# Optimization experiments

Measured on AMD Instinct MI355X. Metric: run time of the kernel, lower is better.

Reference implementation:

```python
import jax, jax.numpy as jnp
import numpy as np

ALPHA = 0.2          # LeakyReLU negative slope
NEG_BIG = -9e15      # zero_vec value used before softmax masking


def setup_inputs() -> dict:
    key = jax.random.key(0)
    k1, k2, k3, k4, k5 = jax.random.split(key, 5)
    N, M, F, K = 2048, 8192, 1024, 10
    feature_matrix = jax.random.normal(k1, (N, F), dtype=jnp.float32)
    embed_matrix = jax.random.normal(k2, (M, F), dtype=jnp.float32)
    # Xavier-ish scaling for params
    weight = jax.random.normal(k3, (F, F), dtype=jnp.float32) * (1.0 / np.sqrt(F))
    a = jax.random.normal(k4, (2 * F, 1), dtype=jnp.float32) * (1.0 / np.sqrt(2 * F))
    neigh_idx = jax.random.randint(k5, (N, K), 0, M, dtype=jnp.int64)
    return {
        "feature_matrix": feature_matrix,
        "embed_matrix": embed_matrix,
        "weight": weight,
        "a": a,
        "neigh_idx": neigh_idx,
    }


def reference(feature_matrix, embed_matrix, weight, a, neigh_idx):
    # feature_matrix: [N, F] features of batch nodes
    # embed_matrix:   [M, F] features of unique sampled neighbors
    # neigh_idx:      [N, K] sampled neighbor columns (set semantics: dups collapse)
    N, F = feature_matrix.shape
    M = embed_matrix.shape[0]
    rows = jnp.arange(N)[:, None]
    mask = jnp.zeros((N, M), dtype=feature_matrix.dtype).at[rows, neigh_idx].set(1.0)

    # GAT kernel path
    hf = feature_matrix @ weight          # [N, F]
    he = embed_matrix @ weight            # [M, F]
    # e_ij = leakyrelu([h_i || h_j] . a) == leakyrelu(h_i.a1 + h_j.a2)
    a1 = a[:F, 0]
    a2 = a[F:, 0]
    e = (hf @ a1)[:, None] + (he @ a2)[None, :]          # [N, M]
    e = jnp.where(e > 0, e, ALPHA * e)                   # LeakyReLU(0.2)
    scores = jnp.where(mask > 0, e, NEG_BIG)
    attention = jax.nn.softmax(scores, axis=1)           # row softmax
    to_feats = attention @ he                            # [N, F]
    return to_feats
```

## Files before the change

### kernel.cpp

```cpp
#include <hip/hip_runtime.h>
#include <math.h>

#define ALPHA 0.2f
#define MAXK 10

typedef _Float16 half8 __attribute__((ext_vector_type(8)));
typedef _Float16 half4 __attribute__((ext_vector_type(4)));
typedef float f32x4 __attribute__((ext_vector_type(4)));

__device__ __forceinline__ void gload_lds16(const void* g, void* l) {
    __builtin_amdgcn_global_load_lds(
        (const __attribute__((address_space(1))) unsigned int*)g,
        (__attribute__((address_space(3))) unsigned int*)l, 16, 0, 0);
}

__global__ void wa_kernel(const float* __restrict__ W, const float* __restrict__ a,
                          float* __restrict__ wa, int F) {
    int wave = (int)((blockIdx.x * blockDim.x + threadIdx.x) >> 6);
    int lane = threadIdx.x & 63;
    if (wave >= F) return;
    const float4* wr = reinterpret_cast<const float4*>(W + (size_t)wave * F);
    const float4* a1 = reinterpret_cast<const float4*>(a);
    const float4* a2 = reinterpret_cast<const float4*>(a + F);
    float acc1 = 0.f, acc2 = 0.f;
    int F4 = F >> 2;
    for (int c = lane; c < F4; c += 64) {
        float4 w = wr[c];
        float4 x = a1[c];
        float4 y = a2[c];
        acc1 += w.x * x.x + w.y * x.y + w.z * x.z + w.w * x.w;
        acc2 += w.x * y.x + w.y * y.y + w.z * y.z + w.w * y.w;
    }
    #pragma unroll
    for (int off = 32; off; off >>= 1) {
        acc1 += __shfl_down(acc1, off);
        acc2 += __shfl_down(acc2, off);
    }
    if (lane == 0) { wa[wave] = acc1; wa[F + wave] = acc2; }
}

__global__ void wt_kernel(const float* __restrict__ W, _Float16* __restrict__ Wt, int F) {
    __shared__ float t[32][33];
    int bx = blockIdx.x * 32;
    int by = blockIdx.y * 32;
    int x = threadIdx.x;
    for (int i = threadIdx.y; i < 32; i += 8)
        t[i][x] = W[(size_t)(bx + i) * F + by + x];
    __syncthreads();
    for (int i = threadIdx.y; i < 32; i += 8)
        Wt[(size_t)(by + i) * F + bx + x] = (_Float16)t[x][i];
}

__global__ __launch_bounds__(256) void aggregate_fused_kernel(
    const float* __restrict__ feat, const float* __restrict__ embed,
    const int* __restrict__ nidx, const float* __restrict__ wa,
    _Float16* __restrict__ agg, int F) {
    const int i = blockIdx.x;
    const int tid = threadIdx.x;
    const int f = tid * 4;

    int idx[MAXK];
    bool dup[MAXK];
    #pragma unroll
    for (int k = 0; k < MAXK; k++) idx[k] = nidx[i * MAXK + k];
    #pragma unroll
    for (int k = 0; k < MAXK; k++) {
        bool d = false;
        #pragma unroll
        for (int p = 0; p < MAXK; p++)
            if (p < k) d |= (idx[p] == idx[k]);
        dup[k] = d;
    }

    float4 wa1 = *(const float4*)&wa[f];
    float4 wa2 = *(const float4*)&wa[F + f];
    float4 fv  = *(const float4*)&feat[(size_t)i * F + f];
    float a1p = fv.x * wa1.x + fv.y * wa1.y + fv.z * wa1.z + fv.w * wa1.w;

    float4 rv[MAXK];
    float a2p[MAXK];
    #pragma unroll
    for (int k = 0; k < MAXK; k++) {
        rv[k] = *(const float4*)&embed[(size_t)idx[k] * F + f];
        a2p[k] = rv[k].x * wa2.x + rv[k].y * wa2.y + rv[k].z * wa2.z + rv[k].w * wa2.w;
    }

    #pragma unroll
    for (int off = 32; off; off >>= 1) {
        a1p += __shfl_down(a1p, off);
        #pragma unroll
        for (int k = 0; k < MAXK; k++) a2p[k] += __shfl_down(a2p[k], off);
    }
    __shared__ float red[MAXK + 1][4];
    const int w = tid >> 6, l = tid & 63;
    if (l == 0) {
        red[0][w] = a1p;
        #pragma unroll
        for (int k = 0; k < MAXK; k++) red[k + 1][w] = a2p[k];
    }
    __syncthreads();

    float s1 = red[0][0] + red[0][1] + red[0][2] + red[0][3];
    float sc[MAXK];
    float m = -INFINITY;
    #pragma unroll
    for (int k = 0; k < MAXK; k++) {
        float v = s1 + red[k + 1][0] + red[k + 1][1] + red[k + 1][2] + red[k + 1][3];
        v = v > 0.f ? v : ALPHA * v;
        sc[k] = v;
        if (!dup[k]) m = fmaxf(m, v);
    }
    float sum = 0.f;
    #pragma unroll
    for (int k = 0; k < MAXK; k++) {
        sc[k] = dup[k] ? 0.f : expf(sc[k] - m);
        sum += sc[k];
    }
    float inv = 1.0f / sum;

    float4 o = make_float4(0.f, 0.f, 0.f, 0.f);
    #pragma unroll
    for (int k = 0; k < MAXK; k++) {
        float wk = sc[k] * inv;
        o.x += wk * rv[k].x;
        o.y += wk * rv[k].y;
        o.z += wk * rv[k].z;
        o.w += wk * rv[k].w;
    }
    half4 h = { (_Float16)o.x, (_Float16)o.y, (_Float16)o.z, (_Float16)o.w };
    *(half4*)&agg[(size_t)i * F + f] = h;
}

__global__ __launch_bounds__(256) void gemm_f16_kernel(
    const _Float16* __restrict__ A, const _Float16* __restrict__ Bt,
    float* __restrict__ C, int M, int N, int K) {
    __shared__ _Float16 As[2][64 * 64];
    __shared__ _Float16 Bs[2][64 * 64];
    const int tid = threadIdx.x;
    const int m0 = blockIdx.y * 64;
    const int n0 = blockIdx.x * 64;
    const int l = tid & 63, wv = tid >> 6;
    const int wm = wv >> 1, wn = wv & 1;
    const int lrow = l & 15, kc = l >> 4;

    const int srow = l >> 3;
    const int sslot = (l & 7) ^ (srow & 7);
    const int nt = K >> 6;

    f32x4 acc[2][2] = {};

    const int rg0 = wv * 2, rg1 = wv * 2 + 1;

    #define STAGE(buf, t)                                                          \
    do {                                                                           \
        int k0_ = (t) * 64;                                                        \
        gload_lds16(&A[(size_t)(m0 + rg0 * 8 + srow) * K + k0_ + sslot * 8],       \
                    (void*)((char*)&As[buf][0] + rg0 * 1024 + l * 16));            \
        gload_lds16(&A[(size_t)(m0 + rg1 * 8 + srow) * K + k0_ + sslot * 8],       \
                    (void*)((char*)&As[buf][0] + rg1 * 1024 + l * 16));            \
        gload_lds16(&Bt[(size_t)(n0 + rg0 * 8 + srow) * K + k0_ + sslot * 8],      \
                    (void*)((char*)&Bs[buf][0] + rg0 * 1024 + l * 16));            \
        gload_lds16(&Bt[(size_t)(n0 + rg1 * 8 + srow) * K + k0_ + sslot * 8],      \
                    (void*)((char*)&Bs[buf][0] + rg1 * 1024 + l * 16));            \
    } while (0)

    STAGE(0, 0);
    asm volatile("s_waitcnt vmcnt(0)" ::: "memory");
    __syncthreads();

    int buf = 0;
    for (int t = 0; t < nt; ++t) {
        if (t + 1 < nt) STAGE(buf ^ 1, t + 1);

        half8 av[2][2], bv[2][2];
        #pragma unroll
        for (int ks = 0; ks < 2; ks++) {
            #pragma unroll
            for (int fq = 0; fq < 2; fq++) {
                int arow = wm * 32 + fq * 16 + lrow;
                int aslot = (ks * 4 + kc) ^ (arow & 7);
                av[ks][fq] = *(const half8*)((const char*)&As[buf][0] + arow * 128 + aslot * 16);
                int brow = wn * 32 + fq * 16 + lrow;
                int bslot = (ks * 4 + kc) ^ (brow & 7);
                bv[ks][fq] = *(const half8*)((const char*)&Bs[buf][0] + brow * 128 + bslot * 16);
            }
        }
        #pragma unroll
        for (int ks = 0; ks < 2; ks++)
            #pragma unroll
            for (int fq = 0; fq < 2; fq++)
                #pragma unroll
                for (int g = 0; g < 2; g++)
                    acc[fq][g] = __builtin_amdgcn_mfma_f32_16x16x32_f16(
                        av[ks][fq], bv[ks][g], acc[fq][g], 0, 0, 0);

        asm volatile("s_waitcnt vmcnt(0)" ::: "memory");
        __syncthreads();
        buf ^= 1;
    }
    #undef STAGE

    #pragma unroll
    for (int fq = 0; fq < 2; fq++)
        #pragma unroll
        for (int g = 0; g < 2; g++)
            #pragma unroll
            for (int r = 0; r < 4; r++)
                C[(size_t)(m0 + wm * 32 + fq * 16 + kc * 4 + r) * N
                  + n0 + wn * 32 + g * 16 + lrow] = acc[fq][g][r];
}

extern "C" void kernel_launch(void* const* d_in, const int* in_sizes, int n_in,
                              void* d_out, int out_size, void* d_ws, size_t ws_size,
                              hipStream_t stream) {
    const float* feat  = (const float*)d_in[0];
    const float* embed = (const float*)d_in[1];
    const float* W     = (const float*)d_in[2];
    const float* a     = (const float*)d_in[3];
    const int*   nidx  = (const int*)d_in[4];

    int F = in_sizes[3] / 2;
    int N = in_sizes[0] / F;
    int M = in_sizes[1] / F;

    float* ws = (float*)d_ws;
    float* wa = ws;
    _Float16* agg_f16 = (_Float16*)(wa + 2 * F);
    _Float16* wt_f16  = agg_f16 + (size_t)N * F;
    (void)M;

    wa_kernel<<<(F * 64 + 255) / 256, 256, 0, stream>>>(W, a, wa, F);
    {
        dim3 grid(F / 32, F / 32), block(32, 8);
        wt_kernel<<<grid, block, 0, stream>>>(W, wt_f16, F);
    }
    aggregate_fused_kernel<<<N, 256, 0, stream>>>(feat, embed, nidx, wa, agg_f16, F);
    {
        dim3 grid(F / 64, N / 64);
        gemm_f16_kernel<<<grid, 256, 0, stream>>>(agg_f16, wt_f16, (float*)d_out, N, F, F);
    }
}
```

Before: 41.41 us.

## Fuse W·a into transpose kernel and enlarge GEMM tile to 128x64 with XCD remap

Folds the W·a reduction into the W transpose kernel. Partial dot products are reduced with 32-lane shuffles and accumulated with atomics after a memset, which removes one kernel launch and a second full read of W. The f16 GEMM tile grows from 64x64 to 128x64, so each wave holds 4x2 MFMA accumulators for more A/B reuse per LDS load. Blocks are also remapped round-robin across 8 XCDs for L2 locality. Costs are float atomics, whose summation order is nondeterministic, higher register and LDS use, and half as many GEMM blocks (256).

```diff
diff --git a/kernel.cpp b/kernel.cpp
--- a/kernel.cpp
+++ b/kernel.cpp
@@ -14,41 +14,31 @@
         (__attribute__((address_space(3))) unsigned int*)l, 16, 0, 0);
 }
 
-__global__ void wa_kernel(const float* __restrict__ W, const float* __restrict__ a,
-                          float* __restrict__ wa, int F) {
-    int wave = (int)((blockIdx.x * blockDim.x + threadIdx.x) >> 6);
-    int lane = threadIdx.x & 63;
-    if (wave >= F) return;
-    const float4* wr = reinterpret_cast<const float4*>(W + (size_t)wave * F);
-    const float4* a1 = reinterpret_cast<const float4*>(a);
-    const float4* a2 = reinterpret_cast<const float4*>(a + F);
-    float acc1 = 0.f, acc2 = 0.f;
-    int F4 = F >> 2;
-    for (int c = lane; c < F4; c += 64) {
-        float4 w = wr[c];
-        float4 x = a1[c];
-        float4 y = a2[c];
-        acc1 += w.x * x.x + w.y * x.y + w.z * x.z + w.w * x.w;
-        acc2 += w.x * y.x + w.y * y.y + w.z * y.z + w.w * y.w;
-    }
-    #pragma unroll
-    for (int off = 32; off; off >>= 1) {
-        acc1 += __shfl_down(acc1, off);
-        acc2 += __shfl_down(acc2, off);
-    }
-    if (lane == 0) { wa[wave] = acc1; wa[F + wave] = acc2; }
-}
-
-__global__ void wt_kernel(const float* __restrict__ W, _Float16* __restrict__ Wt, int F) {
+__global__ void wawt_kernel(const float* __restrict__ W, const float* __restrict__ a,
+                            _Float16* __restrict__ Wt, float* __restrict__ wa, int F) {
     __shared__ float t[32][33];
-    int bx = blockIdx.x * 32;
-    int by = blockIdx.y * 32;
-    int x = threadIdx.x;
-    for (int i = threadIdx.y; i < 32; i += 8)
+    const int bx = blockIdx.x * 32;
+    const int by = blockIdx.y * 32;
+    const int x = threadIdx.x, y = threadIdx.y;
+    for (int i = y; i < 32; i += 8)
         t[i][x] = W[(size_t)(bx + i) * F + by + x];
     __syncthreads();
-    for (int i = threadIdx.y; i < 32; i += 8)
+    for (int i = y; i < 32; i += 8)
         Wt[(size_t)(by + i) * F + bx + x] = (_Float16)t[x][i];
+    float a1 = a[by + x], a2 = a[F + by + x];
+    for (int i = y; i < 32; i += 8) {
+        float w = t[i][x];
+        float p1 = w * a1, p2 = w * a2;
+        #pragma unroll
+        for (int off = 16; off; off >>= 1) {
+            p1 += __shfl_down(p1, off, 32);
+            p2 += __shfl_down(p2, off, 32);
+        }
+        if (x == 0) {
+            atomicAdd(&wa[bx + i], p1);
+            atomicAdd(&wa[F + bx + i], p2);
+        }
+    }
 }
 
 __global__ __launch_bounds__(256) void aggregate_fused_kernel(
@@ -134,34 +124,41 @@
 __global__ __launch_bounds__(256) void gemm_f16_kernel(
     const _Float16* __restrict__ A, const _Float16* __restrict__ Bt,
     float* __restrict__ C, int M, int N, int K) {
-    __shared__ _Float16 As[2][64 * 64];
+    __shared__ _Float16 As[2][128 * 64];
     __shared__ _Float16 Bs[2][64 * 64];
     const int tid = threadIdx.x;
-    const int m0 = blockIdx.y * 64;
-    const int n0 = blockIdx.x * 64;
+
+    int bid = blockIdx.y * gridDim.x + blockIdx.x;
+    int nwg = gridDim.x * gridDim.y;
+    int cpx = nwg >> 3;
+    int wg = (bid & 7) * cpx + (bid >> 3);
+    const int m0 = (wg / gridDim.x) * 128;
+    const int n0 = (wg % gridDim.x) * 64;
+
     const int l = tid & 63, wv = tid >> 6;
     const int wm = wv >> 1, wn = wv & 1;
     const int lrow = l & 15, kc = l >> 4;
-
-    const int srow = l >> 3;
-    const int sslot = (l & 7) ^ (srow & 7);
     const int nt = K >> 6;
 
-    f32x4 acc[2][2] = {};
-
-    const int rg0 = wv * 2, rg1 = wv * 2 + 1;
-
-    #define STAGE(buf, t)                                                          \
-    do {                                                                           \
-        int k0_ = (t) * 64;                                                        \
-        gload_lds16(&A[(size_t)(m0 + rg0 * 8 + srow) * K + k0_ + sslot * 8],       \
-                    (void*)((char*)&As[buf][0] + rg0 * 1024 + l * 16));            \
-        gload_lds16(&A[(size_t)(m0 + rg1 * 8 + srow) * K + k0_ + sslot * 8],       \
-                    (void*)((char*)&As[buf][0] + rg1 * 1024 + l * 16));            \
-        gload_lds16(&Bt[(size_t)(n0 + rg0 * 8 + srow) * K + k0_ + sslot * 8],      \
-                    (void*)((char*)&Bs[buf][0] + rg0 * 1024 + l * 16));            \
-        gload_lds16(&Bt[(size_t)(n0 + rg1 * 8 + srow) * K + k0_ + sslot * 8],      \
-                    (void*)((char*)&Bs[buf][0] + rg1 * 1024 + l * 16));            \
+    f32x4 acc[4][2] = {};
+
+    #define STAGE(buf, t)                                                           \
+    do {                                                                            \
+        int k0_ = (t) * 64;                                                         \
+        _Pragma("unroll")                                                           \
+        for (int r_ = 0; r_ < 4; r_++) {                                            \
+            int u_ = tid + r_ * 256;                                                \
+            int row_ = u_ >> 3, slot_ = (u_ & 7) ^ (row_ & 7);                      \
+            gload_lds16(&A[(size_t)(m0 + row_) * K + k0_ + slot_ * 8],              \
+                        (void*)((char*)&As[buf][0] + u_ * 16));                     \
+        }                                                                           \
+        _Pragma("unroll")                                                           \
+        for (int r_ = 0; r_ < 2; r_++) {                                            \
+            int u_ = tid + r_ * 256;                                                \
+            int row_ = u_ >> 3, slot_ = (u_ & 7) ^ (row_ & 7);                      \
+            gload_lds16(&Bt[(size_t)(n0 + row_) * K + k0_ + slot_ * 8],             \
+                        (void*)((char*)&Bs[buf][0] + u_ * 16));                     \
+        }                                                                           \
     } while (0)
 
     STAGE(0, 0);
@@ -172,27 +169,28 @@
     for (int t = 0; t < nt; ++t) {
         if (t + 1 < nt) STAGE(buf ^ 1, t + 1);
 
-        half8 av[2][2], bv[2][2];
         #pragma unroll
         for (int ks = 0; ks < 2; ks++) {
-            #pragma unroll
-            for (int fq = 0; fq < 2; fq++) {
-                int arow = wm * 32 + fq * 16 + lrow;
+            half8 av[4], bv[2];
+            #pragma unroll
+            for (int fq = 0; fq < 4; fq++) {
+                int arow = wm * 64 + fq * 16 + lrow;
                 int aslot = (ks * 4 + kc) ^ (arow & 7);
-                av[ks][fq] = *(const half8*)((const char*)&As[buf][0] + arow * 128 + aslot * 16);
-                int brow = wn * 32 + fq * 16 + lrow;
+                av[fq] = *(const half8*)((const char*)&As[buf][0] + arow * 128 + aslot * 16);
+            }
+            #pragma unroll
+            for (int g = 0; g < 2; g++) {
+                int brow = wn * 32 + g * 16 + lrow;
                 int bslot = (ks * 4 + kc) ^ (brow & 7);
-                bv[ks][fq] = *(const half8*)((const char*)&Bs[buf][0] + brow * 128 + bslot * 16);
+                bv[g] = *(const half8*)((const char*)&Bs[buf][0] + brow * 128 + bslot * 16);
             }
-        }
-        #pragma unroll
-        for (int ks = 0; ks < 2; ks++)
-            #pragma unroll
-            for (int fq = 0; fq < 2; fq++)
+            #pragma unroll
+            for (int fq = 0; fq < 4; fq++)
                 #pragma unroll
                 for (int g = 0; g < 2; g++)
                     acc[fq][g] = __builtin_amdgcn_mfma_f32_16x16x32_f16(
-                        av[ks][fq], bv[ks][g], acc[fq][g], 0, 0, 0);
+                        av[fq], bv[g], acc[fq][g], 0, 0, 0);
+        }
 
         asm volatile("s_waitcnt vmcnt(0)" ::: "memory");
         __syncthreads();
@@ -201,12 +199,12 @@
     #undef STAGE
 
     #pragma unroll
-    for (int fq = 0; fq < 2; fq++)
+    for (int fq = 0; fq < 4; fq++)
         #pragma unroll
         for (int g = 0; g < 2; g++)
             #pragma unroll
             for (int r = 0; r < 4; r++)
-                C[(size_t)(m0 + wm * 32 + fq * 16 + kc * 4 + r) * N
+                C[(size_t)(m0 + wm * 64 + fq * 16 + kc * 4 + r) * N
                   + n0 + wn * 32 + g * 16 + lrow] = acc[fq][g][r];
 }
 
@@ -229,14 +227,14 @@
     _Float16* wt_f16  = agg_f16 + (size_t)N * F;
     (void)M;
 
-    wa_kernel<<<(F * 64 + 255) / 256, 256, 0, stream>>>(W, a, wa, F);
+    hipMemsetAsync(wa, 0, 2 * F * sizeof(float), stream);
     {
         dim3 grid(F / 32, F / 32), block(32, 8);
-        wt_kernel<<<grid, block, 0, stream>>>(W, wt_f16, F);
+        wawt_kernel<<<grid, block, 0, stream>>>(W, a, wt_f16, wa, F);
     }
     aggregate_fused_kernel<<<N, 256, 0, stream>>>(feat, embed, nidx, wa, agg_f16, F);
     {
-        dim3 grid(F / 64, N / 64);
+        dim3 grid(F / 64, N / 128);
         gemm_f16_kernel<<<grid, 256, 0, stream>>>(agg_f16, wt_f16, (float*)d_out, N, F, F);
     }
 }
```

Result: slower. 53.27 us (+28.7%).

## Merge W transpose into aggregate launch and remap GEMM blocks across XCDs

Applied to the files above, without the earlier changes.

Folds the W-to-f16 transpose into the aggregate kernel as extra trailing blocks, so one kernel launch is removed and the two independent jobs can run concurrently. Separately, the GEMM now remaps its linear block id so consecutive tiles are grouped per XCD (stride-8 interleave), aiming for better L2 reuse of shared A/B tiles. Costs are a branch in the merged kernel, shared-memory usage combined across both paths, and a remap that assumes the block count is divisible by 8.

```diff
diff --git a/kernel.cpp b/kernel.cpp
--- a/kernel.cpp
+++ b/kernel.cpp
@@ -39,24 +39,29 @@
     if (lane == 0) { wa[wave] = acc1; wa[F + wave] = acc2; }
 }
 
-__global__ void wt_kernel(const float* __restrict__ W, _Float16* __restrict__ Wt, int F) {
-    __shared__ float t[32][33];
-    int bx = blockIdx.x * 32;
-    int by = blockIdx.y * 32;
-    int x = threadIdx.x;
-    for (int i = threadIdx.y; i < 32; i += 8)
-        t[i][x] = W[(size_t)(bx + i) * F + by + x];
-    __syncthreads();
-    for (int i = threadIdx.y; i < 32; i += 8)
-        Wt[(size_t)(by + i) * F + bx + x] = (_Float16)t[x][i];
-}
-
-__global__ __launch_bounds__(256) void aggregate_fused_kernel(
+__global__ __launch_bounds__(256) void mid_kernel(
     const float* __restrict__ feat, const float* __restrict__ embed,
     const int* __restrict__ nidx, const float* __restrict__ wa,
-    _Float16* __restrict__ agg, int F) {
+    const float* __restrict__ W, _Float16* __restrict__ agg,
+    _Float16* __restrict__ Wt, int F, int N) {
+    const int tid = threadIdx.x;
+
+    if ((int)blockIdx.x >= N) {
+        __shared__ float t[32][33];
+        const int tb = blockIdx.x - N;
+        const int tpr = F >> 5;
+        const int bx = (tb % tpr) * 32;
+        const int by = (tb / tpr) * 32;
+        const int x = tid & 31, y = tid >> 5;
+        for (int i = y; i < 32; i += 8)
+            t[i][x] = W[(size_t)(bx + i) * F + by + x];
+        __syncthreads();
+        for (int i = y; i < 32; i += 8)
+            Wt[(size_t)(by + i) * F + bx + x] = (_Float16)t[x][i];
+        return;
+    }
+
     const int i = blockIdx.x;
-    const int tid = threadIdx.x;
     const int f = tid * 4;
 
     int idx[MAXK];
@@ -137,8 +142,14 @@
     __shared__ _Float16 As[2][64 * 64];
     __shared__ _Float16 Bs[2][64 * 64];
     const int tid = threadIdx.x;
-    const int m0 = blockIdx.y * 64;
-    const int n0 = blockIdx.x * 64;
+
+    int bid = blockIdx.y * gridDim.x + blockIdx.x;
+    int nwg = gridDim.x * gridDim.y;
+    int cpx = nwg >> 3;
+    int wg = (bid & 7) * cpx + (bid >> 3);
+    const int m0 = (wg / gridDim.x) * 64;
+    const int n0 = (wg % gridDim.x) * 64;
+
     const int l = tid & 63, wv = tid >> 6;
     const int wm = wv >> 1, wn = wv & 1;
     const int lrow = l & 15, kc = l >> 4;
@@ -231,10 +242,10 @@
 
     wa_kernel<<<(F * 64 + 255) / 256, 256, 0, stream>>>(W, a, wa, F);
     {
-        dim3 grid(F / 32, F / 32), block(32, 8);
-        wt_kernel<<<grid, block, 0, stream>>>(W, wt_f16, F);
-    }
-    aggregate_fused_kernel<<<N, 256, 0, stream>>>(feat, embed, nidx, wa, agg_f16, F);
+        int tblocks = (F / 32) * (F / 32);
+        mid_kernel<<<N + tblocks, 256, 0, stream>>>(feat, embed, nidx, wa, W,
+                                                    agg_f16, wt_f16, F, N);
+    }
     {
         dim3 grid(F / 64, N / 64);
         gemm_f16_kernel<<<grid, 256, 0, stream>>>(agg_f16, wt_f16, (float*)d_out, N, F, F);
```

Result: faster. 37.66 us (-9.1%).
